# Kernel tuning notes

Measured on AMD Instinct MI355X. Metric: run time of the kernel, lower is better.

## Reference

```python
import jax, jax.numpy as jnp
import numpy as np

H = 16  # num_attention_heads

def setup_inputs() -> dict:
    key = jax.random.key(0)
    ks = jax.random.split(key, 4)
    B, S, D = 4, 2048, 1024
    scale = 1.0 / np.sqrt(D)
    return {
        "hidden_states": jax.random.normal(ks[0], (B, S, D), dtype=jnp.float32),
        "attention_mask": jnp.zeros((B, 1, 1, S), dtype=jnp.float32),
        "Wq": jax.random.normal(ks[1], (D, D), dtype=jnp.float32) * scale,
        "bq": jnp.zeros((D,), dtype=jnp.float32),
        "Wk": jax.random.normal(ks[2], (D, D), dtype=jnp.float32) * scale,
        "bk": jnp.zeros((D,), dtype=jnp.float32),
        "Wv": jax.random.normal(ks[3], (D, D), dtype=jnp.float32) * scale,
        "bv": jnp.zeros((D,), dtype=jnp.float32),
    }

def _split_heads(x, B, S):
    # [B,S,D] -> [B,H,S,Dh]
    return x.reshape(B, S, H, -1).transpose(0, 2, 1, 3)

def reference(hidden_states, attention_mask, Wq, bq, Wk, bk, Wv, bv):
    B, S, D = hidden_states.shape
    Dh = D // H
    q = _split_heads(hidden_states @ Wq.T + bq, B, S)  # [B,H,S,Dh]
    k = _split_heads(hidden_states @ Wk.T + bk, B, S)
    v = _split_heads(hidden_states @ Wv.T + bv, B, S)
    scores = jnp.einsum("bhqd,bhkd->bhqk", q, k) / jnp.sqrt(jnp.float32(Dh))
    scores = scores + attention_mask  # additive mask, broadcast [B,1,1,S]
    probs = jax.nn.softmax(scores, axis=-1)  # dropout is identity in eval mode
    ctx = jnp.einsum("bhqk,bhkd->bhqd", probs, v)  # [B,H,S,Dh]
    ctx = ctx.transpose(0, 2, 1, 3).reshape(B, S, D)
    return ctx
```

## Files before the change

kernel.cpp:

```cpp
#include <hip/hip_runtime.h>
#include <hip/hip_bf16.h>
#include <stdint.h>

#define LOG2E 1.44269504088896340736f
#define SCL   (0.125f * LOG2E)

typedef __attribute__((ext_vector_type(8)))  short short8;
typedef __attribute__((ext_vector_type(16))) float floatx16;
typedef __attribute__((ext_vector_type(4)))  unsigned short ushort4v;

#define GLP(g, l)                                                              \
    __builtin_amdgcn_global_load_lds(                                          \
        (const __attribute__((address_space(1))) void*)(g),                    \
        (__attribute__((address_space(3))) void*)(l), 16, 0, 0)

#if __has_builtin(__builtin_amdgcn_exp2f)
#define EXP2(x) __builtin_amdgcn_exp2f(x)
#else
#define EXP2(x) exp2f(x)
#endif

static __device__ __forceinline__ unsigned short f2bf(float f) {
    union { float f; unsigned u; } v; v.f = f;
    unsigned r = v.u + 0x7FFFu + ((v.u >> 16) & 1u);
    return (unsigned short)(r >> 16);
}

static __device__ __forceinline__ unsigned pack2bf(float a, float b) {
    __hip_bfloat162 h = __float22bfloat162_rn(make_float2(a, b));
    union { __hip_bfloat162 h; unsigned u; } c; c.h = h; return c.u;
}

#define EXPPACK(dst, sv, base) do {                                            \
        float p0 = EXP2((sv)[(base) + 0]), p1 = EXP2((sv)[(base) + 1]);        \
        float p2 = EXP2((sv)[(base) + 2]), p3 = EXP2((sv)[(base) + 3]);        \
        float p4 = EXP2((sv)[(base) + 4]), p5 = EXP2((sv)[(base) + 5]);        \
        float p6 = EXP2((sv)[(base) + 6]), p7 = EXP2((sv)[(base) + 7]);        \
        dst.uu[0] = pack2bf(p0, p1); dst.uu[1] = pack2bf(p2, p3);              \
        dst.uu[2] = pack2bf(p4, p5); dst.uu[3] = pack2bf(p6, p7);              \
    } while (0)

__global__ __launch_bounds__(256) void cvt_all(const float* __restrict__ X,
                                               const float* __restrict__ Wq,
                                               const float* __restrict__ Wk,
                                               const float* __restrict__ Wv,
                                               const float* __restrict__ mask,
                                               unsigned short* __restrict__ xb,
                                               unsigned short* __restrict__ wb,
                                               float* __restrict__ maskl) {
    int i = blockIdx.x * 256 + threadIdx.x;
    if (i < 2097152) {
        float4 v = ((const float4*)X)[i];
        ushort4v o;
        o.x = f2bf(v.x); o.y = f2bf(v.y); o.z = f2bf(v.z); o.w = f2bf(v.w);
        ((ushort4v*)xb)[i] = o;
    } else if (i < 2883584) {
        int j = i - 2097152;
        const float* src; int k;
        if (j < 262144)      { src = Wq; k = j; }
        else if (j < 524288) { src = Wk; k = j - 262144; }
        else                 { src = Wv; k = j - 524288; }
        float4 v = ((const float4*)src)[k];
        ushort4v o;
        o.x = f2bf(v.x); o.y = f2bf(v.y); o.z = f2bf(v.z); o.w = f2bf(v.w);
        ((ushort4v*)wb)[j] = o;
    } else if (i < 2883584 + 2048) {
        int j = i - 2883584;
        float4 v = ((const float4*)mask)[j];
        ((float4*)maskl)[j] = make_float4(v.x * LOG2E, v.y * LOG2E,
                                          v.z * LOG2E, v.w * LOG2E);
    }
}

__global__ __launch_bounds__(256) void qkv_gemm(
        const unsigned short* __restrict__ X,
        const unsigned short* __restrict__ W,
        const float* __restrict__ bq, const float* __restrict__ bk,
        const float* __restrict__ bv,
        unsigned short* __restrict__ Qf,
        unsigned short* __restrict__ Kf,
        unsigned short* __restrict__ Vt)
{
    __shared__ __align__(16) unsigned short sh[17408];
    unsigned short* Ash = sh;
    unsigned short* Bsh = sh + 8192;

    const int tid  = threadIdx.x;
    const int lane = tid & 63;
    const int wv   = tid >> 6;
    const int q32  = lane & 31;
    const int hi   = lane >> 5;
    const int mBase = blockIdx.x * 128;
    const int nBase = blockIdx.y * 128;
    const int wm = (wv >> 1) * 64;
    const int wn = (wv & 1) * 64;

    floatx16 acc[2][2];
    acc[0][0] = 0.0f; acc[0][1] = 0.0f; acc[1][0] = 0.0f; acc[1][1] = 0.0f;

    const int sr = lane >> 3;
    const int kc = (lane & 7) ^ sr;

    for (int kb = 0; kb < 1024; kb += 64) {
        __syncthreads();
#pragma unroll
        for (int s = 0; s < 4; ++s) {
            const int seg = wv * 4 + s;
            const int row = seg * 8 + sr;
            GLP(X + (size_t)(mBase + row) * 1024 + kb + kc * 8, Ash + seg * 512);
            GLP(W + (size_t)(nBase + row) * 1024 + kb + kc * 8, Bsh + seg * 512);
        }
        __syncthreads();
#pragma unroll
        for (int ks = 0; ks < 4; ++ks) {
            short8 aF[2], bF[2];
#pragma unroll
            for (int mi = 0; mi < 2; ++mi) {
                const int R = wm + mi * 32 + q32;
                const int slot = (2 * ks + hi) ^ (R & 7);
                aF[mi] = *(const short8*)(Ash + (R >> 3) * 512 + (R & 7) * 64 + slot * 8);
            }
#pragma unroll
            for (int ni = 0; ni < 2; ++ni) {
                const int R = wn + ni * 32 + q32;
                const int slot = (2 * ks + hi) ^ (R & 7);
                bF[ni] = *(const short8*)(Bsh + (R >> 3) * 512 + (R & 7) * 64 + slot * 8);
            }
#pragma unroll
            for (int mi = 0; mi < 2; ++mi)
#pragma unroll
                for (int ni = 0; ni < 2; ++ni)
                    acc[mi][ni] = __builtin_amdgcn_mfma_f32_32x32x16_bf16(
                        aF[mi], bF[ni], acc[mi][ni], 0, 0, 0);
        }
    }

    if (blockIdx.y < 16) {
        unsigned short* dst = (blockIdx.y < 8) ? Qf : Kf;
        const float* bias   = (blockIdx.y < 8) ? bq : bk;
        const float scl     = (blockIdx.y < 8) ? SCL : 1.0f;
        const int nb = nBase & 1023;
        float bj[2];
#pragma unroll
        for (int ni = 0; ni < 2; ++ni)
            bj[ni] = bias[nb + wn + ni * 32 + q32];
        __syncthreads();
#pragma unroll
        for (int ni = 0; ni < 2; ++ni) {
            const int col = wn + ni * 32 + q32;
#pragma unroll
            for (int mi = 0; mi < 2; ++mi)
#pragma unroll
                for (int g = 0; g < 4; ++g) {
                    const int row0 = wm + mi * 32 + g * 8 + hi * 4;
#pragma unroll
                    for (int rr = 0; rr < 4; ++rr)
                        sh[(row0 + rr) * 136 + col] =
                            f2bf((acc[mi][ni][g * 4 + rr] + bj[ni]) * scl);
                }
        }
        __syncthreads();
#pragma unroll
        for (int it = 0; it < 8; ++it) {
            const int row  = it * 16 + (tid >> 4);
            const int part = tid & 15;
            short8 v = *(const short8*)(sh + row * 136 + part * 8);
            *(short8*)(dst + (size_t)(mBase + row) * 1024 + nb + part * 8) = v;
        }
    } else {
#pragma unroll
        for (int ni = 0; ni < 2; ++ni) {
            const int gn = nBase + wn + ni * 32 + q32;
            const int c  = gn & 1023;
            const int h  = c >> 6;
            const int d  = c & 63;
            const float bias = bv[c];
#pragma unroll
            for (int mi = 0; mi < 2; ++mi)
#pragma unroll
                for (int g = 0; g < 4; ++g) {
                    const int m0 = mBase + wm + mi * 32 + g * 8 + hi * 4;
                    const int b  = m0 >> 11;
                    const int s0 = m0 & 2047;
                    const int sp = (s0 & ~12) | ((s0 & 4) << 1) | ((s0 & 8) >> 1);
                    ushort4v pv;
#pragma unroll
                    for (int rr = 0; rr < 4; ++rr)
                        pv[rr] = f2bf(acc[mi][ni][g * 4 + rr] + bias);
                    *(ushort4v*)(Vt + (size_t)((b * 16 + h) * 64 + d) * 2048 + sp) = pv;
                }
        }
    }
}

__global__ __launch_bounds__(256)
__attribute__((amdgpu_waves_per_eu(2, 2))) void attn_kernel(
        const unsigned short* __restrict__ Qf,
        const unsigned short* __restrict__ Kf,
        const unsigned short* __restrict__ VT,
        const float* __restrict__ maskl,
        float* __restrict__ out)
{
    __shared__ __align__(16) unsigned short Ksh[2 * 128 * 64];
    __shared__ __align__(16) unsigned short Vsh[2 * 64 * 128];
    __shared__ __align__(16) float Mall[2048];

    const int tid  = threadIdx.x;
    const int lane = tid & 63;
    const int wv   = tid >> 6;
    const int q32  = lane & 31;
    const int hi   = lane >> 5;
    const int bh   = blockIdx.x & 63;
    const int qt   = blockIdx.x >> 6;
    const int b    = bh >> 4;
    const int h    = bh & 15;
    const int q0   = qt * 256 + wv * 64;
    const int sw   = q32 & 7;

    short8 bQ0[4], bQ1[4];
#pragma unroll
    for (int ks = 0; ks < 4; ++ks) {
        bQ0[ks] = *(const short8*)(Qf + (size_t)(b * 2048 + q0 + q32) * 1024
                                      + h * 64 + ks * 16 + hi * 8);
        bQ1[ks] = *(const short8*)(Qf + (size_t)(b * 2048 + q0 + 32 + q32) * 1024
                                      + h * 64 + ks * 16 + hi * 8);
    }

    short8 ones;
#pragma unroll
    for (int j = 0; j < 8; ++j) ones[j] = (short)0x3F80;

    floatx16 accO00 = 0.0f, accO01 = 0.0f;
    floatx16 accO10 = 0.0f, accO11 = 0.0f;
    floatx16 lacc0 = 0.0f, lacc1 = 0.0f;

    const unsigned short* gK = Kf + (size_t)(b * 2048) * 1024 + h * 64;
    const unsigned short* gV = VT + (size_t)(bh * 64) * 2048;
    const float* mrow = maskl + b * 2048;

    const unsigned short* kb4[4];
    const unsigned short* vb4[4];
#pragma unroll
    for (int ks = 0; ks < 4; ++ks) {
        const int cs = (2 * ks + hi) ^ sw;
        kb4[ks] = Ksh + q32 * 64 + cs * 8;
        vb4[ks] = Vsh + q32 * 128 + cs * 8;
    }

    const int krr = lane >> 3;
    const int kcs = lane & 7;
    const int vrr = lane >> 4;
    const int vcs = lane & 15;

    auto STAGE = [&](int kbn, int so) {
#pragma unroll
        for (int s = 0; s < 4; ++s) {
            const int seg = wv * 4 + s;
            const int rK  = seg * 8 + krr;
            const int cK  = kcs ^ (rK & 7);
            GLP(gK + (size_t)(kbn + rK) * 1024 + cK * 8, Ksh + so + seg * 512);
            const int rV  = seg * 4 + vrr;
            const int cV  = vcs ^ (rV & 7);
            GLP(gV + (size_t)rV * 2048 + kbn + cV * 8, Vsh + so + seg * 512);
        }
    };

    auto TILE = [&](int kb, int ro, int so) {
        if (kb + 128 < 2048) STAGE(kb + 128, so);
        const float* mloc = Mall + kb + hi * 4;
#pragma unroll 1
        for (int half = 0; half < 2; ++half) {
            short8 aK0[4], aK1[4];
#pragma unroll
            for (int ks = 0; ks < 4; ++ks) {
                aK0[ks] = *(const short8*)(kb4[ks] + ro + half * 4096);
                aK1[ks] = *(const short8*)(kb4[ks] + ro + half * 4096 + 2048);
            }
            const float* mh = mloc + half * 64;
#pragma unroll
            for (int mt = 0; mt < 2; ++mt) {
                const short8* aK = (mt == 0) ? aK0 : aK1;
                floatx16 mC;
#pragma unroll
                for (int a = 0; a < 4; ++a) {
                    float4 mv = *(const float4*)(mh + mt * 32 + a * 8);
                    mC[4 * a + 0] = mv.x; mC[4 * a + 1] = mv.y;
                    mC[4 * a + 2] = mv.z; mC[4 * a + 3] = mv.w;
                }
                __builtin_amdgcn_s_setprio(1);
                floatx16 s0 = __builtin_amdgcn_mfma_f32_32x32x16_bf16(aK[0], bQ0[0], mC, 0, 0, 0);
                floatx16 s1 = __builtin_amdgcn_mfma_f32_32x32x16_bf16(aK[0], bQ1[0], mC, 0, 0, 0);
#pragma unroll
                for (int ks = 1; ks < 4; ++ks) {
                    s0 = __builtin_amdgcn_mfma_f32_32x32x16_bf16(aK[ks], bQ0[ks], s0, 0, 0, 0);
                    s1 = __builtin_amdgcn_mfma_f32_32x32x16_bf16(aK[ks], bQ1[ks], s1, 0, 0, 0);
                }
                __builtin_amdgcn_s_setprio(0);
                short8 bVa0 = *(const short8*)(vb4[2 * mt + 0] + ro + half * 64);
                short8 bVa1 = *(const short8*)(vb4[2 * mt + 0] + ro + 4096 + half * 64);
                short8 bVb0 = *(const short8*)(vb4[2 * mt + 1] + ro + half * 64);
                short8 bVb1 = *(const short8*)(vb4[2 * mt + 1] + ro + 4096 + half * 64);
                union { unsigned uu[4]; short8 s; } aPa, aPb, aPc, aPd;
                EXPPACK(aPa, s0, 0);
                EXPPACK(aPb, s0, 8);
                EXPPACK(aPc, s1, 0);
                EXPPACK(aPd, s1, 8);
                __builtin_amdgcn_s_setprio(1);
                accO00 = __builtin_amdgcn_mfma_f32_32x32x16_bf16(aPa.s, bVa0, accO00, 0, 0, 0);
                accO01 = __builtin_amdgcn_mfma_f32_32x32x16_bf16(aPa.s, bVa1, accO01, 0, 0, 0);
                lacc0  = __builtin_amdgcn_mfma_f32_32x32x16_bf16(aPa.s, ones, lacc0, 0, 0, 0);
                accO00 = __builtin_amdgcn_mfma_f32_32x32x16_bf16(aPb.s, bVb0, accO00, 0, 0, 0);
                accO01 = __builtin_amdgcn_mfma_f32_32x32x16_bf16(aPb.s, bVb1, accO01, 0, 0, 0);
                lacc0  = __builtin_amdgcn_mfma_f32_32x32x16_bf16(aPb.s, ones, lacc0, 0, 0, 0);
                accO10 = __builtin_amdgcn_mfma_f32_32x32x16_bf16(aPc.s, bVa0, accO10, 0, 0, 0);
                accO11 = __builtin_amdgcn_mfma_f32_32x32x16_bf16(aPc.s, bVa1, accO11, 0, 0, 0);
                lacc1  = __builtin_amdgcn_mfma_f32_32x32x16_bf16(aPc.s, ones, lacc1, 0, 0, 0);
                accO10 = __builtin_amdgcn_mfma_f32_32x32x16_bf16(aPd.s, bVb0, accO10, 0, 0, 0);
                accO11 = __builtin_amdgcn_mfma_f32_32x32x16_bf16(aPd.s, bVb1, accO11, 0, 0, 0);
                lacc1  = __builtin_amdgcn_mfma_f32_32x32x16_bf16(aPd.s, ones, lacc1, 0, 0, 0);
                __builtin_amdgcn_s_setprio(0);
            }
        }
        asm volatile("s_waitcnt vmcnt(0) lgkmcnt(0)" ::: "memory");
        __builtin_amdgcn_s_barrier();
    };

#pragma unroll
    for (int s = 0; s < 2; ++s)
        GLP(mrow + (wv * 2 + s) * 256 + lane * 4, Mall + (wv * 2 + s) * 256);
    STAGE(0, 0);
    asm volatile("s_waitcnt vmcnt(0)" ::: "memory");
    __builtin_amdgcn_s_barrier();

#pragma unroll 1
    for (int kb2 = 0; kb2 < 2048; kb2 += 256) {
        TILE(kb2,       0,    8192);
        TILE(kb2 + 128, 8192, 0);
    }

#pragma unroll
    for (int g = 0; g < 4; ++g)
#pragma unroll
        for (int rr = 0; rr < 4; ++rr) {
            const int r   = g * 4 + rr;
            const int row = rr + 8 * g + 4 * hi;
            const float li0 = 1.0f / lacc0[r];
            const float li1 = 1.0f / lacc1[r];
            float* op0 = out + (size_t)(b * 2048 + q0 + row) * 1024 + h * 64 + q32;
            float* op1 = out + (size_t)(b * 2048 + q0 + 32 + row) * 1024 + h * 64 + q32;
            op0[0]  = accO00[r] * li0;
            op0[32] = accO01[r] * li0;
            op1[0]  = accO10[r] * li1;
            op1[32] = accO11[r] * li1;
        }
}

extern "C" void kernel_launch(void* const* d_in, const int* in_sizes, int n_in,
                              void* d_out, int out_size, void* d_ws, size_t ws_size,
                              hipStream_t stream) {
    const float* X    = (const float*)d_in[0];
    const float* mask = (const float*)d_in[1];
    const float* Wq   = (const float*)d_in[2];
    const float* bq   = (const float*)d_in[3];
    const float* Wk   = (const float*)d_in[4];
    const float* bk   = (const float*)d_in[5];
    const float* Wv   = (const float*)d_in[6];
    const float* bv   = (const float*)d_in[7];
    float* out = (float*)d_out;

    char* ws = (char*)d_ws;
    unsigned short* xb  = (unsigned short*)(ws);
    unsigned short* wb  = (unsigned short*)(ws + 16777216);
    unsigned short* qf  = (unsigned short*)(ws + 23068672);
    unsigned short* kf  = (unsigned short*)(ws + 39845888);
    unsigned short* vtb = (unsigned short*)(ws + 56623104);
    float*          ml  = (float*)(ws + 73400320);

    cvt_all<<<11272, 256, 0, stream>>>(X, Wq, Wk, Wv, mask, xb, wb, ml);

    qkv_gemm<<<dim3(64, 24), 256, 0, stream>>>(xb, wb, bq, bk, bv, qf, kf, vtb);

    attn_kernel<<<512, 256, 0, stream>>>(qf, kf, vtb, ml, out);
}
```

Before: 242.0 us.

## Enlarge QKV GEMM tiles to 256x256 with 512 threads and double-buffered LDS

```diff
diff --git a/kernel.cpp b/kernel.cpp
--- a/kernel.cpp
+++ b/kernel.cpp
@@ -72,7 +72,8 @@
     }
 }
 
-__global__ __launch_bounds__(256) void qkv_gemm(
+__global__ __launch_bounds__(512)
+__attribute__((amdgpu_waves_per_eu(2, 2))) void qkv_gemm(
         const unsigned short* __restrict__ X,
         const unsigned short* __restrict__ W,
         const float* __restrict__ bq, const float* __restrict__ bk,
@@ -81,102 +82,124 @@
         unsigned short* __restrict__ Kf,
         unsigned short* __restrict__ Vt)
 {
-    __shared__ __align__(16) unsigned short sh[17408];
-    unsigned short* Ash = sh;
-    unsigned short* Bsh = sh + 8192;
+    __shared__ __align__(16) unsigned short AB[65536];
 
     const int tid  = threadIdx.x;
     const int lane = tid & 63;
     const int wv   = tid >> 6;
     const int q32  = lane & 31;
     const int hi   = lane >> 5;
-    const int mBase = blockIdx.x * 128;
-    const int nBase = blockIdx.y * 128;
-    const int wm = (wv >> 1) * 64;
-    const int wn = (wv & 1) * 64;
-
-    floatx16 acc[2][2];
-    acc[0][0] = 0.0f; acc[0][1] = 0.0f; acc[1][0] = 0.0f; acc[1][1] = 0.0f;
+    const int sw   = q32 & 7;
+    const int mBase = blockIdx.x * 256;
+    const int nBase = blockIdx.y * 256;
+    const int wm = (wv >> 2) * 128;
+    const int wn = (wv & 3) * 64;
+
+    floatx16 acc[4][2];
+#pragma unroll
+    for (int mi = 0; mi < 4; ++mi) { acc[mi][0] = 0.0f; acc[mi][1] = 0.0f; }
 
     const int sr = lane >> 3;
     const int kc = (lane & 7) ^ sr;
 
-    for (int kb = 0; kb < 1024; kb += 64) {
-        __syncthreads();
-#pragma unroll
-        for (int s = 0; s < 4; ++s) {
-            const int seg = wv * 4 + s;
+    const unsigned short* aBase[4];
+    const unsigned short* bBase[4];
+#pragma unroll
+    for (int ks = 0; ks < 4; ++ks) {
+        const int cs = ((2 * ks + hi) ^ sw) * 8;
+        aBase[ks] = AB + ((wv >> 2) * 16 + (q32 >> 3)) * 512 + sw * 64 + cs;
+        bBase[ks] = AB + 32768 + ((wv & 3) * 8 + (q32 >> 3)) * 512 + sw * 64 + cs;
+    }
+
+    auto STAGE = [&](int kb, int so) {
+#pragma unroll
+        for (int r = 0; r < 4; ++r) {
+            const int seg = r * 8 + wv;
             const int row = seg * 8 + sr;
-            GLP(X + (size_t)(mBase + row) * 1024 + kb + kc * 8, Ash + seg * 512);
-            GLP(W + (size_t)(nBase + row) * 1024 + kb + kc * 8, Bsh + seg * 512);
-        }
-        __syncthreads();
-#pragma unroll
-        for (int ks = 0; ks < 4; ++ks) {
-            short8 aF[2], bF[2];
-#pragma unroll
-            for (int mi = 0; mi < 2; ++mi) {
-                const int R = wm + mi * 32 + q32;
-                const int slot = (2 * ks + hi) ^ (R & 7);
-                aF[mi] = *(const short8*)(Ash + (R >> 3) * 512 + (R & 7) * 64 + slot * 8);
+            GLP(X + (size_t)(mBase + row) * 1024 + kb + kc * 8, AB + so + seg * 512);
+            GLP(W + (size_t)(nBase + row) * 1024 + kb + kc * 8, AB + 32768 + so + seg * 512);
+        }
+    };
+
+    STAGE(0, 0);
+    asm volatile("s_waitcnt vmcnt(0)" ::: "memory");
+    __builtin_amdgcn_s_barrier();
+
+#pragma unroll 1
+    for (int t = 0; t < 16; ++t) {
+        const int so  = (t & 1) * 16384;
+        if (t < 15) STAGE((t + 1) * 64, ((t + 1) & 1) * 16384);
+        short8 bF[2][4];
+#pragma unroll
+        for (int ni = 0; ni < 2; ++ni)
+#pragma unroll
+            for (int ks = 0; ks < 4; ++ks)
+                bF[ni][ks] = *(const short8*)(bBase[ks] + so + ni * 2048);
+#pragma unroll
+        for (int mi = 0; mi < 4; ++mi) {
+            short8 aF[4];
+#pragma unroll
+            for (int ks = 0; ks < 4; ++ks)
+                aF[ks] = *(const short8*)(aBase[ks] + so + mi * 2048);
+#pragma unroll
+            for (int ks = 0; ks < 4; ++ks) {
+                acc[mi][0] = __builtin_amdgcn_mfma_f32_32x32x16_bf16(
+                    aF[ks], bF[0][ks], acc[mi][0], 0, 0, 0);
+                acc[mi][1] = __builtin_amdgcn_mfma_f32_32x32x16_bf16(
+                    aF[ks], bF[1][ks], acc[mi][1], 0, 0, 0);
             }
-#pragma unroll
-            for (int ni = 0; ni < 2; ++ni) {
-                const int R = wn + ni * 32 + q32;
-                const int slot = (2 * ks + hi) ^ (R & 7);
-                bF[ni] = *(const short8*)(Bsh + (R >> 3) * 512 + (R & 7) * 64 + slot * 8);
-            }
-#pragma unroll
-            for (int mi = 0; mi < 2; ++mi)
-#pragma unroll
-                for (int ni = 0; ni < 2; ++ni)
-                    acc[mi][ni] = __builtin_amdgcn_mfma_f32_32x32x16_bf16(
-                        aF[mi], bF[ni], acc[mi][ni], 0, 0, 0);
-        }
-    }
-
-    if (blockIdx.y < 16) {
-        unsigned short* dst = (blockIdx.y < 8) ? Qf : Kf;
-        const float* bias   = (blockIdx.y < 8) ? bq : bk;
-        const float scl     = (blockIdx.y < 8) ? SCL : 1.0f;
+        }
+        asm volatile("s_waitcnt vmcnt(0) lgkmcnt(0)" ::: "memory");
+        __builtin_amdgcn_s_barrier();
+    }
+
+    if (blockIdx.y < 8) {
+        unsigned short* dst = (blockIdx.y < 4) ? Qf : Kf;
+        const float* bias   = (blockIdx.y < 4) ? bq : bk;
+        const float scl     = (blockIdx.y < 4) ? SCL : 1.0f;
         const int nb = nBase & 1023;
         float bj[2];
 #pragma unroll
         for (int ni = 0; ni < 2; ++ni)
             bj[ni] = bias[nb + wn + ni * 32 + q32];
-        __syncthreads();
+#pragma unroll 1
+        for (int hh = 0; hh < 2; ++hh) {
+            if ((wm >> 7) == hh) {
+#pragma unroll
+                for (int ni = 0; ni < 2; ++ni) {
+                    const int col = wn + ni * 32 + q32;
+#pragma unroll
+                    for (int mi = 0; mi < 4; ++mi)
+#pragma unroll
+                        for (int g = 0; g < 4; ++g) {
+                            const int row0 = mi * 32 + g * 8 + hi * 4;
+#pragma unroll
+                            for (int rr = 0; rr < 4; ++rr)
+                                AB[(row0 + rr) * 264 + col] =
+                                    f2bf((acc[mi][ni][g * 4 + rr] + bj[ni]) * scl);
+                        }
+                }
+            }
+            __syncthreads();
+#pragma unroll
+            for (int it = 0; it < 8; ++it) {
+                const int row  = it * 16 + (tid >> 5);
+                const int part = tid & 31;
+                short8 v = *(const short8*)(AB + row * 264 + part * 8);
+                *(short8*)(dst + (size_t)(mBase + hh * 128 + row) * 1024
+                               + nb + part * 8) = v;
+            }
+            __syncthreads();
+        }
+    } else {
 #pragma unroll
         for (int ni = 0; ni < 2; ++ni) {
-            const int col = wn + ni * 32 + q32;
-#pragma unroll
-            for (int mi = 0; mi < 2; ++mi)
-#pragma unroll
-                for (int g = 0; g < 4; ++g) {
-                    const int row0 = wm + mi * 32 + g * 8 + hi * 4;
-#pragma unroll
-                    for (int rr = 0; rr < 4; ++rr)
-                        sh[(row0 + rr) * 136 + col] =
-                            f2bf((acc[mi][ni][g * 4 + rr] + bj[ni]) * scl);
-                }
-        }
-        __syncthreads();
-#pragma unroll
-        for (int it = 0; it < 8; ++it) {
-            const int row  = it * 16 + (tid >> 4);
-            const int part = tid & 15;
-            short8 v = *(const short8*)(sh + row * 136 + part * 8);
-            *(short8*)(dst + (size_t)(mBase + row) * 1024 + nb + part * 8) = v;
-        }
-    } else {
-#pragma unroll
-        for (int ni = 0; ni < 2; ++ni) {
-            const int gn = nBase + wn + ni * 32 + q32;
-            const int c  = gn & 1023;
-            const int h  = c >> 6;
-            const int d  = c & 63;
+            const int c = (nBase - 2048) + wn + ni * 32 + q32;
+            const int h = c >> 6;
+            const int d = c & 63;
             const float bias = bv[c];
 #pragma unroll
-            for (int mi = 0; mi < 2; ++mi)
+            for (int mi = 0; mi < 4; ++mi)
 #pragma unroll
                 for (int g = 0; g < 4; ++g) {
                     const int m0 = mBase + wm + mi * 32 + g * 8 + hi * 4;
@@ -378,7 +401,7 @@
 
     cvt_all<<<11272, 256, 0, stream>>>(X, Wq, Wk, Wv, mask, xb, wb, ml);
 
-    qkv_gemm<<<dim3(64, 24), 256, 0, stream>>>(xb, wb, bq, bk, bv, qf, kf, vtb);
+    qkv_gemm<<<dim3(32, 12), 512, 0, stream>>>(xb, wb, bq, bk, bv, qf, kf, vtb);
 
     attn_kernel<<<512, 256, 0, stream>>>(qf, kf, vtb, ml, out);
 }
```

After: 243.8 us. About the same (+0.7%).
